# Kernel optimization log

Hardware: AMD Instinct MI355X
Metric: run time of the kernel (lower is better)

Reference implementation:

```python
import jax, jax.numpy as jnp
import numpy as np

N, E = 50000, 1600000
DIN, DOUT, H, DG = 128, 128, 8, 64
DH = DOUT // H  # per-head dim
NEG_SLOPE = 0.2


def _leaky(x):
    return jnp.where(x >= 0, x, NEG_SLOPE * x)


def setup_inputs() -> dict:
    key = jax.random.key(0)
    ks = jax.random.split(key, 9)
    row = jax.random.randint(ks[0], (E,), 0, N, dtype=jnp.int32)
    col = jax.random.randint(ks[1], (E,), 0, N, dtype=jnp.int32)
    val = jax.random.uniform(ks[2], (E,), dtype=jnp.float32)  # normalized adj values
    feat = jax.random.normal(ks[3], (N, DIN), dtype=jnp.float32)
    W = jax.random.normal(ks[4], (2, H, DIN, DH), dtype=jnp.float32) * 0.05
    b = jnp.zeros((2, H, DH), dtype=jnp.float32)
    att = jax.random.normal(ks[5], (H, 2 * DH), dtype=jnp.float32) * 0.1
    offset = jnp.zeros((2, DOUT), dtype=jnp.float32)
    scale = jnp.ones((2, DOUT), dtype=jnp.float32)
    weight_gate = jax.random.normal(ks[6], (2 * DIN + DG, H), dtype=jnp.float32) * 0.05
    weight_pool_gate = jax.random.normal(ks[7], (DIN, DG), dtype=jnp.float32) * 0.05
    return {"row": row, "col": col, "val": val, "feat": feat, "W": W, "b": b,
            "att": att, "offset": offset, "scale": scale,
            "weight_gate": weight_gate, "weight_pool_gate": weight_pool_gate}


def reference(row, col, val, feat, W, b, att, offset, scale, weight_gate, weight_pool_gate):
    # ---- gate values (GaAN eq. 3) ----
    zj = feat @ weight_pool_gate                                   # [N, DG]
    zmax = jax.ops.segment_max(zj[col], row, num_segments=N)       # max-pool over neighbors
    zmax = jnp.where(jnp.isfinite(zmax), zmax, 0.0)                # isolated nodes -> 0
    nmean = jax.ops.segment_sum(val[:, None] * feat[col], row, num_segments=N)  # spmm(adj, feat)
    gate = jnp.concatenate([feat, zmax, nmean], axis=1) @ weight_gate            # [N, H]
    # ---- per-order, per-head linear + relu ----
    fp = jax.nn.relu(jnp.einsum('nd,ohdk->onhk', feat, W) + b[:, None])  # [2, N, H, DH]
    f0, f1 = fp[0], fp[1]                                          # self / neighbor feats
    # ---- attention-weighted sparse aggregation ----
    a_self = _leaky(jnp.einsum('nhk,hk->nh', f0, att[:, :DH]))     # [N, H]
    a_neigh = _leaky(jnp.einsum('nhk,hk->nh', f1, att[:, DH:]))    # [N, H]
    w_edge = (a_self[row] + a_neigh[col]) * val[:, None]           # [E, H]
    agg = jax.ops.segment_sum(w_edge[:, :, None] * f1[col], row, num_segments=N)  # [N, H, DH]
    agg = agg * gate[:, :, None]                                   # gated heads
    h0 = f0.reshape(N, DOUT)
    h1 = agg.reshape(N, DOUT)
    # ---- per-node norm (torch _batch_norm over feature dim) ----
    def norm(x, s, o):
        mu = jnp.mean(x, axis=1, keepdims=True)
        var = jnp.var(x, axis=1, keepdims=True) + 1e-9
        return (x - mu) * s * jax.lax.rsqrt(var) + o
    h0 = norm(h0, scale[0], offset[0])
    h1 = norm(h1, scale[1], offset[1])
    return h0 + h1  # aggr == 'mean'
```

## Files before the change

### kernel.cpp

```cpp
#include <hip/hip_runtime.h>
#include <hip/hip_bf16.h>
#include <math.h>

#define DIN   128
#define DOUTC 128
#define HH    8
#define DHH   16
#define DGG   64
#define NC2   352
#define PH    176
#define PT    11
#define BSHIFT 7
#define CAP   6144
#define HB    64
#define EPB   4096

typedef __attribute__((ext_vector_type(8))) short short8v;
typedef __attribute__((ext_vector_type(4))) float float4v;

__global__ __launch_bounds__(256) void setup_kernel(
    const float* __restrict__ feat, const float* __restrict__ W, const float* __restrict__ b,
    const float* __restrict__ Wg, const float* __restrict__ Wpg, const int* __restrict__ row,
    __hip_bfloat16* __restrict__ featb, __hip_bfloat16* __restrict__ Btb, float* __restrict__ biasv,
    int* __restrict__ gHistP, int total8, int cvtB, int prepB, int E, int EH) {
    int bid = blockIdx.x, tid = threadIdx.x;
    if (bid < cvtB) {
        int i = bid * 256 + tid;
        if (i < total8) {
            const float4* p = reinterpret_cast<const float4*>(feat) + 2 * (size_t)i;
            float4 x = p[0], y = p[1];
            union { __hip_bfloat16 h[8]; short8v v; } pk;
            pk.h[0] = __float2bfloat16(x.x); pk.h[1] = __float2bfloat16(x.y);
            pk.h[2] = __float2bfloat16(x.z); pk.h[3] = __float2bfloat16(x.w);
            pk.h[4] = __float2bfloat16(y.x); pk.h[5] = __float2bfloat16(y.y);
            pk.h[6] = __float2bfloat16(y.z); pk.h[7] = __float2bfloat16(y.w);
            reinterpret_cast<short8v*>(featb)[i] = pk.v;
        }
    } else if (bid < cvtB + prepB) {
        int idx = (bid - cvtB) * 256 + tid;
        if (idx < NC2 * DIN) {
            int col = idx >> 7;
            int k   = idx & 127;
            float v = 0.f;
            if (col < 256) {
                int o = col >> 7, jj = col & 127, h = jj >> 4, kd = jj & 15;
                v = W[((o * HH + h) * DIN + k) * DHH + kd];
            } else if (col < 320) {
                v = Wpg[k * DGG + (col - 256)];
            } else if (col < 328) {
                v = Wg[k * HH + (col - 320)];
            } else if (col < 336) {
                v = Wg[(192 + k) * HH + (col - 328)];
            }
            int u = (k >> 3) ^ (col & 7);
            Btb[col * DIN + u * 8 + (k & 7)] = __float2bfloat16(v);
        }
        if (idx < NC2) {
            float bv = 0.f;
            if (idx < 256) { int o = idx >> 7, jj = idx & 127; bv = b[(o * HH + (jj >> 4)) * DHH + (jj & 15)]; }
            biasv[idx] = bv;
        }
    } else {
        __shared__ int hist[512];
        int hb = bid - cvtB - prepB;
        hist[tid] = 0; hist[tid + 256] = 0;
        __syncthreads();
        int e0 = hb * EH, e1 = e0 + EH; if (e1 > E) e1 = E;
        for (int e = e0 + tid; e < e1; e += 256) atomicAdd(&hist[row[e] >> BSHIFT], 1);
        __syncthreads();
        gHistP[hb * 512 + tid] = hist[tid];
        gHistP[hb * 512 + tid + 256] = hist[tid + 256];
    }
}

__global__ __launch_bounds__(256, 1) void dense_mfma(
    const __hip_bfloat16* __restrict__ featb, const __hip_bfloat16* __restrict__ Btb,
    const float* __restrict__ biasv,
    float* __restrict__ f0, __hip_bfloat16* __restrict__ f1b, __hip_bfloat16* __restrict__ zjb,
    float* __restrict__ fg0, float* __restrict__ nodedat, int N) {
    __shared__ __align__(16) __hip_bfloat16 Bs[PH * DIN];
    int t   = threadIdx.x;
    int wid = t >> 6, l = t & 63;
    int r0  = blockIdx.x * 128 + wid * 32;
    int lr  = l & 15;
    int lk  = l >> 4;

    short8v a[2][4];
    #pragma unroll
    for (int rt = 0; rt < 2; ++rt) {
        int node = r0 + rt * 16 + lr;
        if (node >= N) node = N - 1;
        const short8v* ap = reinterpret_cast<const short8v*>(&featb[(size_t)node * DIN + lk * 8]);
        #pragma unroll
        for (int kk = 0; kk < 4; ++kk) a[rt][kk] = ap[kk * 4];
    }

    #pragma unroll
    for (int p = 0; p < 2; ++p) {
        __syncthreads();
        {
            const short8v* src = reinterpret_cast<const short8v*>(Btb + (size_t)p * PH * DIN);
            short8v* dst = reinterpret_cast<short8v*>(Bs);
            #pragma unroll
            for (int it = 0; it < 11; ++it) dst[it * 256 + t] = src[it * 256 + t];
        }
        __syncthreads();

        float4v acc[2][PT];
        #pragma unroll
        for (int rt = 0; rt < 2; ++rt)
            #pragma unroll
            for (int n = 0; n < PT; ++n) acc[rt][n] = (float4v)0.f;

        #pragma unroll
        for (int n = 0; n < PT; ++n) {
            int coll = n * 16 + lr;
            #pragma unroll
            for (int kk = 0; kk < 4; ++kk) {
                int u = (kk * 4 + lk) ^ (lr & 7);
                short8v bv = *reinterpret_cast<const short8v*>(&Bs[coll * DIN + u * 8]);
                acc[0][n] = __builtin_amdgcn_mfma_f32_16x16x32_bf16(a[0][kk], bv, acc[0][n], 0, 0, 0);
                acc[1][n] = __builtin_amdgcn_mfma_f32_16x16x32_bf16(a[1][kk], bv, acc[1][n], 0, 0, 0);
            }
        }

        #pragma unroll
        for (int rt = 0; rt < 2; ++rt) {
            #pragma unroll
            for (int rg = 0; rg < 4; ++rg) {
                int node = r0 + rt * 16 + lk * 4 + rg;
                if (node < N) {
                    #pragma unroll
                    for (int n = 0; n < PT; ++n) {
                        int col = p * PH + n * 16 + lr;
                        float v = acc[rt][n][rg] + biasv[col];
                        if (col < 128) {
                            v = v > 0.f ? v : 0.f;
                            f0[(size_t)node * DOUTC + col] = v;
                        } else if (col < 256) {
                            v = v > 0.f ? v : 0.f;
                            f1b[(size_t)node * DOUTC + (col - 128)] = __float2bfloat16(v);
                        } else if (col < 320) {
                            zjb[(size_t)node * DGG + (col - 256)] = __float2bfloat16(v);
                        } else if (col < 328) {
                            fg0[node * HH + (col - 320)] = v;
                        } else if (col < 336) {
                            nodedat[(size_t)node * 16 + 8 + (col - 328)] = v;
                        }
                    }
                }
            }
        }
    }
}

__global__ __launch_bounds__(512) void mid_kernel(
    const float* __restrict__ f0, const __hip_bfloat16* __restrict__ f1b,
    const float* __restrict__ att, float* __restrict__ a_self, float* __restrict__ nodedat,
    const int* __restrict__ gHistP, int* __restrict__ gHist, int* __restrict__ gBase,
    int* __restrict__ gCursor, int N, int attnB) {
    int bid = blockIdx.x, tid = threadIdx.x;
    if (bid < attnB) {
        int g = bid * 512 + tid;
        if (g >= N * 16) return;
        int node = g >> 4, u = g & 15, h = u >> 1;
        float s = 0.f;
        if ((u & 1) == 0) {
            const float4* p  = reinterpret_cast<const float4*>(&f0[(size_t)node * DOUTC + h * DHH]);
            const float*  av = &att[h * 32];
            #pragma unroll
            for (int q = 0; q < 4; ++q) {
                float4 x = p[q];
                s = fmaf(x.x, av[q * 4 + 0], fmaf(x.y, av[q * 4 + 1],
                    fmaf(x.z, av[q * 4 + 2], fmaf(x.w, av[q * 4 + 3], s))));
            }
            s = (s >= 0.f) ? s : 0.2f * s;
            a_self[node * HH + h] = s;
        } else {
            const short8v* p = reinterpret_cast<const short8v*>(&f1b[(size_t)node * DOUTC + h * DHH]);
            const float*  av = &att[h * 32 + DHH];
            union { short8v v; __hip_bfloat16 hh[8]; } pk0, pk1;
            pk0.v = p[0]; pk1.v = p[1];
            #pragma unroll
            for (int q = 0; q < 8; ++q) s = fmaf(__bfloat162float(pk0.hh[q]), av[q], s);
            #pragma unroll
            for (int q = 0; q < 8; ++q) s = fmaf(__bfloat162float(pk1.hh[q]), av[8 + q], s);
            s = (s >= 0.f) ? s : 0.2f * s;
            nodedat[(size_t)node * 16 + h] = s;
        }
    } else {
        __shared__ int s[512];
        int v = 0;
        #pragma unroll
        for (int s8 = 0; s8 < HB; ++s8) v += gHistP[s8 * 512 + tid];
        gHist[tid] = v;
        s[tid] = v; __syncthreads();
        for (int off = 1; off < 512; off <<= 1) {
            int add = (tid >= off) ? s[tid - off] : 0;
            __syncthreads();
            s[tid] += add;
            __syncthreads();
        }
        int excl = s[tid] - v;
        gBase[tid] = excl;
        gCursor[tid] = excl;
    }
}

__global__ __launch_bounds__(256) void bscatter(const int* __restrict__ row, const int* __restrict__ col,
                                                const float* __restrict__ val, int* __restrict__ gCursor,
                                                int2* __restrict__ ebuf, int E) {
    __shared__ int hist[512], base[512], rank[512];
    int tid = threadIdx.x;
    hist[tid] = 0; hist[tid + 256] = 0;
    __syncthreads();
    int e0 = blockIdx.x * EPB;
    #pragma unroll
    for (int k = 0; k < 16; ++k) {
        int e = e0 + k * 256 + tid;
        if (e < E) atomicAdd(&hist[row[e] >> BSHIFT], 1);
    }
    __syncthreads();
    if (hist[tid])       base[tid] = atomicAdd(&gCursor[tid], hist[tid]);
    if (hist[tid + 256]) base[tid + 256] = atomicAdd(&gCursor[tid + 256], hist[tid + 256]);
    rank[tid] = 0; rank[tid + 256] = 0;
    __syncthreads();
    #pragma unroll
    for (int k = 0; k < 16; ++k) {
        int e = e0 + k * 256 + tid;
        if (e < E) {
            int r = row[e];
            int bk = r >> BSHIFT;
            int loc = atomicAdd(&rank[bk], 1);
            int2 pk;
            pk.x = col[e] | ((r & 127) << 16);
            pk.y = __float_as_int(val[e]);
            ebuf[base[bk] + loc] = pk;
        }
    }
}

__global__ __launch_bounds__(256) void bsort(const int2* __restrict__ ebuf, const int* __restrict__ gHist,
                                             const int* __restrict__ gBase, int2* __restrict__ efin,
                                             int* __restrict__ rowptr, int N) {
    __shared__ int2 ent[CAP];
    __shared__ int h0[128], sc[128], rk[128];
    int b = blockIdx.x, tid = threadIdx.x;
    int cnt = gHist[b]; if (cnt > CAP) cnt = CAP;
    int base = gBase[b];
    if (tid < 128) h0[tid] = 0;
    __syncthreads();
    for (int i = tid; i < cnt; i += 256) {
        int2 e = ebuf[base + i];
        ent[i] = e;
        atomicAdd(&h0[(e.x >> 16) & 127], 1);
    }
    __syncthreads();
    if (tid < 128) sc[tid] = h0[tid];
    __syncthreads();
    for (int off = 1; off < 128; off <<= 1) {
        int add = (tid < 128 && tid >= off) ? sc[tid - off] : 0;
        __syncthreads();
        if (tid < 128) sc[tid] += add;
        __syncthreads();
    }
    if (tid < 128) {
        int excl = sc[tid] - h0[tid];
        rk[tid] = excl;
        int grow = b * 128 + tid;
        if (grow <= N) rowptr[grow] = base + excl;
    }
    __syncthreads();
    for (int i = tid; i < cnt; i += 256) {
        int2 e = ent[i];
        int dst = base + atomicAdd(&rk[(e.x >> 16) & 127], 1);
        efin[dst] = e;
    }
}

#define UN 8
__global__ __launch_bounds__(128) void edge_kernel(
    const int* __restrict__ rowptr, const int2* __restrict__ ef,
    const __hip_bfloat16* __restrict__ f1b, const __hip_bfloat16* __restrict__ zjb,
    const float* __restrict__ a_self, const float* __restrict__ nodedat,
    const float* __restrict__ fg0, const float* __restrict__ Wg,
    const float* __restrict__ f0, const float* __restrict__ scale, const float* __restrict__ offset,
    float* __restrict__ out) {
    int r = blockIdx.x;
    int t = threadIdx.x;
    int start = rowptr[r], end = rowptr[r + 1];

    __shared__ float lds_z[64];
    __shared__ float lds_n8[8];
    __shared__ float lds_gate[8];

    float accA0 = 0.f, accA1 = 0.f, accZ = -INFINITY, accN8 = 0.f;
    int h = t >> 3;
    float asr = 0.f;
    if (t < 64) asr = a_self[r * HH + h];
    int j = t - 64;

    int i = start;
    for (; i + UN <= end; i += UN) {
        int   c[UN]; float v[UN];
        #pragma unroll
        for (int u = 0; u < UN; ++u) {
            int2 eu = ef[i + u];
            c[u] = eu.x & 0xFFFF;
            v[u] = __int_as_float(eu.y);
        }
        if (t < 64) {
            float an[UN];
            #pragma unroll
            for (int u = 0; u < UN; ++u) an[u] = nodedat[(size_t)c[u] * 16 + h];
            __hip_bfloat162 f2[UN];
            #pragma unroll
            for (int u = 0; u < UN; ++u)
                f2[u] = *reinterpret_cast<const __hip_bfloat162*>(&f1b[(size_t)c[u] * DOUTC + 2 * t]);
            #pragma unroll
            for (int u = 0; u < UN; ++u) {
                float w = (asr + an[u]) * v[u];
                accA0 = fmaf(w, __bfloat162float(f2[u].x), accA0);
                accA1 = fmaf(w, __bfloat162float(f2[u].y), accA1);
            }
        } else {
            float z[UN];
            #pragma unroll
            for (int u = 0; u < UN; ++u) z[u] = __bfloat162float(zjb[(size_t)c[u] * DGG + j]);
            #pragma unroll
            for (int u = 0; u < UN; ++u) accZ = fmaxf(accZ, z[u]);
            if (j < 8) {
                float g2[UN];
                #pragma unroll
                for (int u = 0; u < UN; ++u) g2[u] = nodedat[(size_t)c[u] * 16 + 8 + j];
                #pragma unroll
                for (int u = 0; u < UN; ++u) accN8 = fmaf(v[u], g2[u], accN8);
            }
        }
    }
    for (; i < end; ++i) {
        int2 eu = ef[i];
        int   c = eu.x & 0xFFFF;
        float v = __int_as_float(eu.y);
        if (t < 64) {
            float w = (asr + nodedat[(size_t)c * 16 + h]) * v;
            __hip_bfloat162 f2 = *reinterpret_cast<const __hip_bfloat162*>(&f1b[(size_t)c * DOUTC + 2 * t]);
            accA0 = fmaf(w, __bfloat162float(f2.x), accA0);
            accA1 = fmaf(w, __bfloat162float(f2.y), accA1);
        } else {
            accZ = fmaxf(accZ, __bfloat162float(zjb[(size_t)c * DGG + j]));
            if (j < 8) accN8 = fmaf(v, nodedat[(size_t)c * 16 + 8 + j], accN8);
        }
    }

    if (t >= 64) {
        lds_z[j] = (end > start) ? accZ : 0.f;
        if (j < 8) lds_n8[j] = accN8;
    }
    __syncthreads();

    if (t < 8) {
        float g = fg0[r * HH + t] + lds_n8[t];
        #pragma unroll
        for (int k = 0; k < 64; ++k) g = fmaf(lds_z[k], Wg[(128 + k) * HH + t], g);
        lds_gate[t] = g;
    }
    __syncthreads();

    if (t < 64) {
        float gh  = lds_gate[h];
        float h1x = accA0 * gh, h1y = accA1 * gh;
        float2 f0v = *reinterpret_cast<const float2*>(&f0[r * DOUTC + 2 * t]);
        float s0  = f0v.x + f0v.y;
        float s0q = f0v.x * f0v.x + f0v.y * f0v.y;
        float s1  = h1x + h1y;
        float s1q = h1x * h1x + h1y * h1y;
        #pragma unroll
        for (int off = 32; off > 0; off >>= 1) {
            s0  += __shfl_xor(s0,  off);
            s0q += __shfl_xor(s0q, off);
            s1  += __shfl_xor(s1,  off);
            s1q += __shfl_xor(s1q, off);
        }
        float mu0  = s0 * (1.f / 128.f), mu1 = s1 * (1.f / 128.f);
        float rs0  = rsqrtf(s0q * (1.f / 128.f) - mu0 * mu0 + 1e-9f);
        float rs1  = rsqrtf(s1q * (1.f / 128.f) - mu1 * mu1 + 1e-9f);
        float2 sc0 = *reinterpret_cast<const float2*>(&scale[2 * t]);
        float2 sc1 = *reinterpret_cast<const float2*>(&scale[128 + 2 * t]);
        float2 of0 = *reinterpret_cast<const float2*>(&offset[2 * t]);
        float2 of1 = *reinterpret_cast<const float2*>(&offset[128 + 2 * t]);
        float2 o2;
        o2.x = (f0v.x - mu0) * sc0.x * rs0 + of0.x + (h1x - mu1) * sc1.x * rs1 + of1.x;
        o2.y = (f0v.y - mu0) * sc0.y * rs0 + of0.y + (h1y - mu1) * sc1.y * rs1 + of1.y;
        *reinterpret_cast<float2*>(&out[r * DOUTC + 2 * t]) = o2;
    }
}

extern "C" void kernel_launch(void* const* d_in, const int* in_sizes, int n_in,
                              void* d_out, int out_size, void* d_ws, size_t ws_size,
                              hipStream_t stream) {
    const int*   row  = (const int*)  d_in[0];
    const int*   col  = (const int*)  d_in[1];
    const float* val  = (const float*)d_in[2];
    const float* feat = (const float*)d_in[3];
    const float* W    = (const float*)d_in[4];
    const float* b    = (const float*)d_in[5];
    const float* att  = (const float*)d_in[6];
    const float* offs = (const float*)d_in[7];
    const float* scal = (const float*)d_in[8];
    const float* Wg   = (const float*)d_in[9];
    const float* Wpg  = (const float*)d_in[10];
    float* out = (float*)d_out;

    const int E = in_sizes[0];
    const int N = in_sizes[3] / DIN;
    const int NBUCK = (N + 127) >> BSHIFT;
    const int NEBLK = (E + EPB - 1) / EPB;

    char* ws = (char*)d_ws;
    size_t off = 0;
    auto alloc = [&](size_t bytes) { size_t o = off; off = (off + bytes + 255) & ~(size_t)255; return o; };

    __hip_bfloat16* featb = (__hip_bfloat16*)(ws + alloc((size_t)N * DIN * 2));
    __hip_bfloat16* Btb   = (__hip_bfloat16*)(ws + alloc((size_t)NC2 * DIN * 2));
    float* biasv   = (float*)(ws + alloc(NC2 * 4));
    float* f0      = (float*)(ws + alloc((size_t)N * DOUTC * 4));
    __hip_bfloat16* f1b = (__hip_bfloat16*)(ws + alloc((size_t)N * DOUTC * 2));
    __hip_bfloat16* zjb = (__hip_bfloat16*)(ws + alloc((size_t)N * DGG * 2));
    float* a_self  = (float*)(ws + alloc((size_t)N * HH * 4));
    float* nodedat = (float*)(ws + alloc((size_t)N * 16 * 4));
    float* fg0     = (float*)(ws + alloc((size_t)N * HH * 4));
    int*   rowptr  = (int*)  (ws + alloc((size_t)(N + 1) * 4));
    int*   gHistP  = (int*)  (ws + alloc((size_t)HB * 512 * 4));
    int*   gHist   = (int*)  (ws + alloc(512 * 4));
    int*   gBase   = (int*)  (ws + alloc(512 * 4));
    int*   gCursor = (int*)  (ws + alloc(512 * 4));
    int2*  ebuf    = (int2*) (ws + alloc((size_t)E * 8));
    int2*  efin    = (int2*) (ws + alloc((size_t)E * 8));

    const int total8 = N * DIN / 8;
    const int cvtB = (total8 + 255) / 256;
    const int prepB = (NC2 * DIN + 255) / 256;
    const int EH = (E + HB - 1) / HB;
    setup_kernel<<<cvtB + prepB + HB, 256, 0, stream>>>(
        feat, W, b, Wg, Wpg, row, featb, Btb, biasv, gHistP, total8, cvtB, prepB, E, EH);
    dense_mfma<<<(N + 127) / 128, 256, 0, stream>>>(featb, Btb, biasv, f0, f1b, zjb, fg0, nodedat, N);
    const int attnB = (N * 16 + 511) / 512;
    mid_kernel<<<attnB + 1, 512, 0, stream>>>(f0, f1b, att, a_self, nodedat,
                                              gHistP, gHist, gBase, gCursor, N, attnB);
    bscatter<<<NEBLK, 256, 0, stream>>>(row, col, val, gCursor, ebuf, E);
    bsort<<<NBUCK, 256, 0, stream>>>(ebuf, gHist, gBase, efin, rowptr, N);
    edge_kernel<<<N, 128, 0, stream>>>(rowptr, efin, f1b, zjb, a_self, nodedat,
                                       fg0, Wg, f0, scal, offs, out);
}
```

Baseline: 341.8 us.

## Store nodedat in bf16, relax dense launch bounds, split edge kernel launch

Stores the per-node neighbor attention scores and the gate projection terms (nodedat) as bf16 instead of fp32. This halves the bytes fetched per edge in the gather-heavy edge kernel. It also drops the min-blocks hint on dense_mfma and splits the edge kernel into two launches over halves of the nodes. The bf16 storage loses precision in the attention and gate terms, and the split adds one extra launch.

New measurement: 347.3 us. No clear change (+1.6%).

```diff
diff --git a/kernel.cpp b/kernel.cpp
--- a/kernel.cpp
+++ b/kernel.cpp
@@ -73,11 +73,11 @@
     }
 }
 
-__global__ __launch_bounds__(256, 1) void dense_mfma(
+__global__ __launch_bounds__(256) void dense_mfma(
     const __hip_bfloat16* __restrict__ featb, const __hip_bfloat16* __restrict__ Btb,
     const float* __restrict__ biasv,
     float* __restrict__ f0, __hip_bfloat16* __restrict__ f1b, __hip_bfloat16* __restrict__ zjb,
-    float* __restrict__ fg0, float* __restrict__ nodedat, int N) {
+    float* __restrict__ fg0, __hip_bfloat16* __restrict__ nodedat, int N) {
     __shared__ __align__(16) __hip_bfloat16 Bs[PH * DIN];
     int t   = threadIdx.x;
     int wid = t >> 6, l = t & 63;
@@ -145,7 +145,7 @@
                         } else if (col < 328) {
                             fg0[node * HH + (col - 320)] = v;
                         } else if (col < 336) {
-                            nodedat[(size_t)node * 16 + 8 + (col - 328)] = v;
+                            nodedat[(size_t)node * 16 + 8 + (col - 328)] = __float2bfloat16(v);
                         }
                     }
                 }
@@ -156,7 +156,7 @@
 
 __global__ __launch_bounds__(512) void mid_kernel(
     const float* __restrict__ f0, const __hip_bfloat16* __restrict__ f1b,
-    const float* __restrict__ att, float* __restrict__ a_self, float* __restrict__ nodedat,
+    const float* __restrict__ att, float* __restrict__ a_self, __hip_bfloat16* __restrict__ nodedat,
     const int* __restrict__ gHistP, int* __restrict__ gHist, int* __restrict__ gBase,
     int* __restrict__ gCursor, int N, int attnB) {
     int bid = blockIdx.x, tid = threadIdx.x;
@@ -186,7 +186,7 @@
             #pragma unroll
             for (int q = 0; q < 8; ++q) s = fmaf(__bfloat162float(pk1.hh[q]), av[8 + q], s);
             s = (s >= 0.f) ? s : 0.2f * s;
-            nodedat[(size_t)node * 16 + h] = s;
+            nodedat[(size_t)node * 16 + h] = __float2bfloat16(s);
         }
     } else {
         __shared__ int s[512];
@@ -282,11 +282,11 @@
 __global__ __launch_bounds__(128) void edge_kernel(
     const int* __restrict__ rowptr, const int2* __restrict__ ef,
     const __hip_bfloat16* __restrict__ f1b, const __hip_bfloat16* __restrict__ zjb,
-    const float* __restrict__ a_self, const float* __restrict__ nodedat,
+    const float* __restrict__ a_self, const __hip_bfloat16* __restrict__ nodedat,
     const float* __restrict__ fg0, const float* __restrict__ Wg,
     const float* __restrict__ f0, const float* __restrict__ scale, const float* __restrict__ offset,
-    float* __restrict__ out) {
-    int r = blockIdx.x;
+    float* __restrict__ out, int rbase) {
+    int r = rbase + blockIdx.x;
     int t = threadIdx.x;
     int start = rowptr[r], end = rowptr[r + 1];
 
@@ -312,7 +312,7 @@
         if (t < 64) {
             float an[UN];
             #pragma unroll
-            for (int u = 0; u < UN; ++u) an[u] = nodedat[(size_t)c[u] * 16 + h];
+            for (int u = 0; u < UN; ++u) an[u] = __bfloat162float(nodedat[(size_t)c[u] * 16 + h]);
             __hip_bfloat162 f2[UN];
             #pragma unroll
             for (int u = 0; u < UN; ++u)
@@ -332,7 +332,7 @@
             if (j < 8) {
                 float g2[UN];
                 #pragma unroll
-                for (int u = 0; u < UN; ++u) g2[u] = nodedat[(size_t)c[u] * 16 + 8 + j];
+                for (int u = 0; u < UN; ++u) g2[u] = __bfloat162float(nodedat[(size_t)c[u] * 16 + 8 + j]);
                 #pragma unroll
                 for (int u = 0; u < UN; ++u) accN8 = fmaf(v[u], g2[u], accN8);
             }
@@ -343,13 +343,13 @@
         int   c = eu.x & 0xFFFF;
         float v = __int_as_float(eu.y);
         if (t < 64) {
-            float w = (asr + nodedat[(size_t)c * 16 + h]) * v;
+            float w = (asr + __bfloat162float(nodedat[(size_t)c * 16 + h])) * v;
             __hip_bfloat162 f2 = *reinterpret_cast<const __hip_bfloat162*>(&f1b[(size_t)c * DOUTC + 2 * t]);
             accA0 = fmaf(w, __bfloat162float(f2.x), accA0);
             accA1 = fmaf(w, __bfloat162float(f2.y), accA1);
         } else {
             accZ = fmaxf(accZ, __bfloat162float(zjb[(size_t)c * DGG + j]));
-            if (j < 8) accN8 = fmaf(v, nodedat[(size_t)c * 16 + 8 + j], accN8);
+            if (j < 8) accN8 = fmaf(v, __bfloat162float(nodedat[(size_t)c * 16 + 8 + j]), accN8);
         }
     }
 
@@ -428,7 +428,7 @@
     __hip_bfloat16* f1b = (__hip_bfloat16*)(ws + alloc((size_t)N * DOUTC * 2));
     __hip_bfloat16* zjb = (__hip_bfloat16*)(ws + alloc((size_t)N * DGG * 2));
     float* a_self  = (float*)(ws + alloc((size_t)N * HH * 4));
-    float* nodedat = (float*)(ws + alloc((size_t)N * 16 * 4));
+    __hip_bfloat16* nodedat = (__hip_bfloat16*)(ws + alloc((size_t)N * 16 * 2));
     float* fg0     = (float*)(ws + alloc((size_t)N * HH * 4));
     int*   rowptr  = (int*)  (ws + alloc((size_t)(N + 1) * 4));
     int*   gHistP  = (int*)  (ws + alloc((size_t)HB * 512 * 4));
@@ -450,6 +450,9 @@
                                               gHistP, gHist, gBase, gCursor, N, attnB);
     bscatter<<<NEBLK, 256, 0, stream>>>(row, col, val, gCursor, ebuf, E);
     bsort<<<NBUCK, 256, 0, stream>>>(ebuf, gHist, gBase, efin, rowptr, N);
-    edge_kernel<<<N, 128, 0, stream>>>(rowptr, efin, f1b, zjb, a_self, nodedat,
-                                       fg0, Wg, f0, scal, offs, out);
-}
+    int half = N / 2;
+    edge_kernel<<<half, 128, 0, stream>>>(rowptr, efin, f1b, zjb, a_self, nodedat,
+                                          fg0, Wg, f0, scal, offs, out, 0);
+    edge_kernel<<<N - half, 128, 0, stream>>>(rowptr, efin, f1b, zjb, a_self, nodedat,
+                                              fg0, Wg, f0, scal, offs, out, half);
+}
```
